# Optimization experiments

Hardware: AMD Instinct MI355X
Metric: run time of the kernel (lower is better)

The kernel has to match this reference:

```python
import jax, jax.numpy as jnp
import numpy as np

B, IN, OUT, K = 2048, 1024, 1024, 20


def setup_inputs() -> dict:
    key = jax.random.key(0)
    k1, k2 = jax.random.split(key)
    x = jax.random.normal(k1, (B, IN), dtype=jnp.float32)
    # per-output, per-input spline coefficients: (out_features, in_features, num_knots)
    W = jax.random.normal(k2, (OUT, IN, K), dtype=jnp.float32) * 0.1
    # evenly spaced knot grid on [-2, 2] (linspace)
    knots = jnp.linspace(-2.0, 2.0, K, dtype=jnp.float32)
    return {"x": x, "W": W, "knots": knots}


def reference(x, W, knots):
    # RBF spline basis shared across all output features (this is the fusion
    # the original per-output Python loop misses):
    # basis[b, i, k] = exp(-0.5 * ((x[b, i] - knots[k]) / h)^2)
    h = knots[1] - knots[0]  # uniform knot spacing -> RBF bandwidth
    basis = jnp.exp(-0.5 * jnp.square((x[:, :, None] - knots) / h))  # (B, IN, K)
    # Each SplineLayer o computes sum_{i,k} W[o,i,k] * basis[b,i,k]; the
    # KANBlock concatenates the OUT scalars -> a single einsum.
    return jnp.einsum("bik,oik->bo", basis, W)  # (B, OUT)
```

## Files before the change

kernel.cpp:

```cpp
#include <hip/hip_runtime.h>

#define B_DIM 2048
#define IN_DIM 1024
#define OUT_DIM 1024
#define K_KNOTS 20
#define KR (IN_DIM * K_KNOTS)
#define OUT_ELEMS (B_DIM * OUT_DIM)

#define TM 128
#define TN 128
#define BK 128
#define KSPLIT 4
#define MT_TILES (B_DIM / TM)
#define NT_TILES (OUT_DIM / TN)
#define GEMM_BLOCKS (MT_TILES * NT_TILES * KSPLIT)
#define LDS_AS0 0
#define LDS_AS1 8192
#define LDS_BS0 16384
#define LDS_BS1 24576

#define NB_QUADS (B_DIM * IN_DIM * 5)
#define NB_BASIS_BLK (NB_QUADS / 256)
#define NW4 (OUT_DIM * KR / 8)
#define NB_W_BLK (NW4 / 256)

typedef __bf16 bf16x8 __attribute__((ext_vector_type(8)));
typedef float  f32x4  __attribute__((ext_vector_type(4)));

#define MFMA16(a, b, c) __builtin_amdgcn_mfma_f32_16x16x32_bf16(a, b, c, 0, 0, 0)

__device__ __forceinline__ unsigned short f2bf(float f) {
    unsigned int u = __float_as_uint(f);
    unsigned int r = u + 0x7fffu + ((u >> 16) & 1u);
    return (unsigned short)(r >> 16);
}

__device__ __forceinline__ unsigned int pack2(float lo, float hi) {
    return (unsigned int)f2bf(lo) | ((unsigned int)f2bf(hi) << 16);
}

__device__ __forceinline__ void async_load16(const void* g, void* l) {
    __builtin_amdgcn_global_load_lds(
        (const __attribute__((address_space(1))) void*)g,
        (__attribute__((address_space(3))) void*)l,
        16, 0, 0);
}

__global__ void zero_out_kernel(float* out) {
    int idx = (blockIdx.x * 256 + threadIdx.x) * 4;
    float4 z = {0.f, 0.f, 0.f, 0.f};
    *(float4*)(out + idx) = z;
}

__global__ void __launch_bounds__(256) prep_kernel(
        const float* __restrict__ x,
        const float4* __restrict__ Wsrc,
        const float* __restrict__ knots,
        uint2* __restrict__ basis_out,
        uint4* __restrict__ w_out) {
    if (blockIdx.x < NB_BASIS_BLK) {
        unsigned int n = blockIdx.x * 256 + threadIdx.x;
        unsigned int q  = n % 5u;
        unsigned int bi = n / 5u;
        float t0 = knots[0];
        float h  = knots[1] - t0;
        float invh = 1.0f / h;
        float xv = x[bi];
        float k0 = (float)(4 * q);
        float v[4];
#pragma unroll
        for (int j = 0; j < 4; ++j) {
            float t = __builtin_fmaf(k0 + (float)j, h, t0);
            float d = (xv - t) * invh;
            v[j] = __expf(-0.5f * d * d);
        }
        uint2 o;
        o.x = pack2(v[0], v[1]);
        o.y = pack2(v[2], v[3]);
        basis_out[n] = o;
    } else {
        unsigned int t = (blockIdx.x - NB_BASIS_BLK) * 256 + threadIdx.x;
        float4 a = Wsrc[2 * t];
        float4 b = Wsrc[2 * t + 1];
        uint4 o;
        o.x = pack2(a.x, a.y);
        o.y = pack2(a.z, a.w);
        o.z = pack2(b.x, b.y);
        o.w = pack2(b.z, b.w);
        w_out[t] = o;
    }
}

#define AOFF(s, h) (((s) * 2 + (h)) * 8192)
#define BOFF(s, h) (32768 + ((s) * 2 + (h)) * 8192)

template <int S>
__device__ __forceinline__ void tile_step(
        int t, int ntiles,
        const unsigned short* __restrict__ Ab,
        const unsigned short* __restrict__ Bb,
        unsigned short* lds,
        f32x4 (&acc)[8][4],
        int m0, int n0, int k0,
        int wave, int wm, int wn, int r15, int c0, int c1,
        int srow8, int scol) {
    const int aB  = S * 16384 + (wm * 128 + r15) * 64;
    const int bB  = 32768 + S * 16384 + (wn * 64 + r15) * 64;
    const int kb1 = k0 + (t + 1) * 64;
    const bool st = (t + 1 < ntiles);

    auto stage = [&](const unsigned short* __restrict__ src, int grow, int kb, int lbase) {
        const unsigned short* g = src + (size_t)(grow + wave * 16 + srow8) * KR + kb + scol;
        async_load16(g,                  &lds[lbase + wave * 1024]);
        async_load16(g + (size_t)8 * KR, &lds[lbase + wave * 1024 + 512]);
    };

    bf16x8 a0[4], a1[4], b0[4], b1[4], s0[4], s1[4];

#pragma unroll
    for (int i = 0; i < 4; ++i) a0[i] = *(const bf16x8*)&lds[aB + i * 1024 + c0];
#pragma unroll
    for (int j = 0; j < 4; ++j) b0[j] = *(const bf16x8*)&lds[bB + j * 1024 + c0];
    __builtin_amdgcn_s_barrier();
    asm volatile("s_waitcnt lgkmcnt(0)" ::: "memory");
    __builtin_amdgcn_sched_barrier(0);
    __builtin_amdgcn_s_setprio(1);
#pragma unroll
    for (int i = 0; i < 4; ++i)
#pragma unroll
        for (int j = 0; j < 4; ++j)
            acc[i][j] = MFMA16(a0[i], b0[j], acc[i][j]);
    __builtin_amdgcn_s_setprio(0);

#pragma unroll
    for (int i = 0; i < 4; ++i) a1[i] = *(const bf16x8*)&lds[aB + i * 1024 + c1];
#pragma unroll
    for (int j = 0; j < 4; ++j) b1[j] = *(const bf16x8*)&lds[bB + j * 1024 + c1];
    __builtin_amdgcn_s_barrier();
    asm volatile("s_waitcnt lgkmcnt(0)" ::: "memory");
    __builtin_amdgcn_sched_barrier(0);
    __builtin_amdgcn_s_setprio(1);
#pragma unroll
    for (int i = 0; i < 4; ++i)
#pragma unroll
        for (int j = 0; j < 4; ++j)
            acc[i][j] = MFMA16(a1[i], b1[j], acc[i][j]);
    __builtin_amdgcn_s_setprio(0);

#pragma unroll
    for (int i = 0; i < 4; ++i) s0[i] = *(const bf16x8*)&lds[aB + (4 + i) * 1024 + c0];
    if (st) {
        stage(Ab, m0,       kb1, AOFF(S ^ 1, 0));
        stage(Ab, m0 + 128, kb1, AOFF(S ^ 1, 1));
    }
    __builtin_amdgcn_s_barrier();
    asm volatile("s_waitcnt lgkmcnt(0)" ::: "memory");
    __builtin_amdgcn_sched_barrier(0);
    __builtin_amdgcn_s_setprio(1);
#pragma unroll
    for (int i = 0; i < 4; ++i)
#pragma unroll
        for (int j = 0; j < 4; ++j)
            acc[4 + i][j] = MFMA16(s0[i], b0[j], acc[4 + i][j]);
    __builtin_amdgcn_s_setprio(0);

#pragma unroll
    for (int i = 0; i < 4; ++i) s1[i] = *(const bf16x8*)&lds[aB + (4 + i) * 1024 + c1];
    if (st) {
        stage(Bb, n0,       kb1, BOFF(S ^ 1, 0));
        stage(Bb, n0 + 128, kb1, BOFF(S ^ 1, 1));
    }
    __builtin_amdgcn_s_barrier();
    asm volatile("s_waitcnt lgkmcnt(0)" ::: "memory");
    __builtin_amdgcn_sched_barrier(0);
    __builtin_amdgcn_s_setprio(1);
#pragma unroll
    for (int i = 0; i < 4; ++i)
#pragma unroll
        for (int j = 0; j < 4; ++j)
            acc[4 + i][j] = MFMA16(s1[i], b1[j], acc[4 + i][j]);
    __builtin_amdgcn_s_setprio(0);

    if (st) asm volatile("s_waitcnt vmcnt(0)" ::: "memory");
    __builtin_amdgcn_s_barrier();
}

template <int KS, bool ATOMIC>
__global__ void __launch_bounds__(512, 2)
kan_gemm8(const unsigned short* __restrict__ Ab,
          const unsigned short* __restrict__ Bb,
          float* __restrict__ out) {
    __shared__ __align__(16) unsigned short lds[65536];

    constexpr int KPBk   = KR / KS;
    constexpr int NTILES = KPBk / 64;

    const int id  = blockIdx.x;
    const int z   = id & 7;
    const int ord = id >> 3;
    const int mt  = ord & 7;
    const int nt  = ord >> 3;
    const int m0  = mt * 256;
    const int n0  = nt * 256;
    const int k0  = z * KPBk;

    const int tid  = threadIdx.x;
    const int wave = tid >> 6;
    const int lane = tid & 63;
    const int wm   = wave >> 2;
    const int wn   = wave & 3;

    const int srow8 = lane >> 3;
    const int scol  = ((lane & 7) ^ srow8) * 8;

    auto stage = [&](const unsigned short* __restrict__ src, int grow, int kb, int lbase) {
        const unsigned short* g = src + (size_t)(grow + wave * 16 + srow8) * KR + kb + scol;
        async_load16(g,                  &lds[lbase + wave * 1024]);
        async_load16(g + (size_t)8 * KR, &lds[lbase + wave * 1024 + 512]);
    };

    f32x4 acc[8][4];
#pragma unroll
    for (int i = 0; i < 8; ++i)
#pragma unroll
        for (int j = 0; j < 4; ++j) acc[i][j] = (f32x4){0.f, 0.f, 0.f, 0.f};

    const int q   = lane >> 4;
    const int r15 = lane & 15;
    const int r7  = lane & 7;
    const int c0  = (q ^ r7) * 8;
    const int c1  = ((4 + q) ^ r7) * 8;

    stage(Ab, m0,       k0, AOFF(0, 0));
    stage(Ab, m0 + 128, k0, AOFF(0, 1));
    stage(Bb, n0,       k0, BOFF(0, 0));
    stage(Bb, n0 + 128, k0, BOFF(0, 1));
    asm volatile("s_waitcnt vmcnt(0)" ::: "memory");
    __builtin_amdgcn_s_barrier();

    for (int tt = 0; tt < NTILES; tt += 2) {
        tile_step<0>(tt,     NTILES, Ab, Bb, lds, acc, m0, n0, k0,
                     wave, wm, wn, r15, c0, c1, srow8, scol);
        tile_step<1>(tt + 1, NTILES, Ab, Bb, lds, acc, m0, n0, k0,
                     wave, wm, wn, r15, c0, c1, srow8, scol);
    }

    float* dst = ATOMIC ? out : out + (size_t)z * OUT_ELEMS;
#pragma unroll
    for (int i = 0; i < 8; ++i)
#pragma unroll
        for (int j = 0; j < 4; ++j)
#pragma unroll
            for (int r = 0; r < 4; ++r) {
                const int row = m0 + wm * 128 + i * 16 + q * 4 + r;
                const int c   = n0 + wn * 64  + j * 16 + r15;
                if (ATOMIC)
                    atomicAdd(&dst[(size_t)row * OUT_DIM + c], acc[i][j][r]);
                else
                    dst[(size_t)row * OUT_DIM + c] = acc[i][j][r];
            }
}

template <int KS, bool ATOMIC>
__global__ void __launch_bounds__(256)
kan_gemm(const unsigned short* __restrict__ Ab,
         const unsigned short* __restrict__ Bb,
         float* __restrict__ out) {
    __shared__ __align__(16) unsigned short lds[32768];

    const int KPBk = KR / KS;
    const int id   = blockIdx.x;
    const int xcd  = id & 7;
    const int ord  = id >> 3;
    const int mt   = xcd * 2 + (ord & 1);
    const int nt   = (ord >> 1) & (NT_TILES - 1);
    const int z    = ord >> 4;
    const int m0 = mt * TM;
    const int n0 = nt * TN;
    const int k0 = z * KPBk;

    const int tid  = threadIdx.x;
    const int wave = tid >> 6;
    const int lane = tid & 63;
    const int wm = wave & 1;
    const int wn = wave >> 1;

    const int srow = lane >> 3;
    const int scol = ((lane & 7) ^ srow) * 8;

    f32x4 acc[4][4];
#pragma unroll
    for (int i = 0; i < 4; ++i)
#pragma unroll
        for (int j = 0; j < 4; ++j) acc[i][j] = (f32x4){0.f, 0.f, 0.f, 0.f};

    for (int kt = 0; kt < KPBk; kt += BK) {
        const int kb = k0 + kt;
        __syncthreads();
#pragma unroll
        for (int c = 0; c < 4; ++c) {
            const int chunk = wave * 4 + c;
            const int r = chunk * 8 + srow;
            const unsigned short* arow = Ab + (size_t)(m0 + r) * KR + kb + scol;
            const unsigned short* brow = Bb + (size_t)(n0 + r) * KR + kb + scol;
            unsigned short* slot = &lds[chunk * 512];
            async_load16(arow,      slot + LDS_AS0);
            async_load16(arow + 64, slot + LDS_AS1);
            async_load16(brow,      slot + LDS_BS0);
            async_load16(brow + 64, slot + LDS_BS1);
        }
        __syncthreads();

        const int quad = lane >> 4;
        const int r15  = lane & 15;
        const int r7   = lane & 7;
#pragma unroll
        for (int s = 0; s < 4; ++s) {
            const int abase = (s >> 1) ? LDS_AS1 : LDS_AS0;
            const int bbase = (s >> 1) ? LDS_BS1 : LDS_BS0;
            const int cg = (s & 1) * 4 + quad;
            const int xo = (cg ^ r7) * 8;
            bf16x8 af[4], bfv[4];
#pragma unroll
            for (int i = 0; i < 4; ++i) {
                af[i]  = *(const bf16x8*)&lds[abase + (wm * 64 + i * 16 + r15) * 64 + xo];
                bfv[i] = *(const bf16x8*)&lds[bbase + (wn * 64 + i * 16 + r15) * 64 + xo];
            }
#pragma unroll
            for (int i = 0; i < 4; ++i)
#pragma unroll
                for (int j = 0; j < 4; ++j)
                    acc[i][j] = MFMA16(af[i], bfv[j], acc[i][j]);
        }
    }

    float* dst = ATOMIC ? out : out + (size_t)z * OUT_ELEMS;
    const int quad = lane >> 4;
    const int col  = lane & 15;
#pragma unroll
    for (int i = 0; i < 4; ++i)
#pragma unroll
        for (int j = 0; j < 4; ++j)
#pragma unroll
            for (int r = 0; r < 4; ++r) {
                const int row = m0 + wm * 64 + i * 16 + quad * 4 + r;
                const int c   = n0 + wn * 64 + j * 16 + col;
                if (ATOMIC)
                    atomicAdd(&dst[(size_t)row * OUT_DIM + c], acc[i][j][r]);
                else
                    dst[(size_t)row * OUT_DIM + c] = acc[i][j][r];
            }
}

template <int KS>
__global__ void kan_reduce(const float* __restrict__ part, float* __restrict__ out) {
    const int idx = (blockIdx.x * 256 + threadIdx.x) * 4;
    f32x4 s = *(const f32x4*)(part + idx);
#pragma unroll
    for (int z = 1; z < KS; ++z)
        s += *(const f32x4*)(part + (size_t)z * OUT_ELEMS + idx);
    *(f32x4*)(out + idx) = s;
}

__global__ void kan_fallback(const float* __restrict__ x,
                             const float* __restrict__ W,
                             const float* __restrict__ knots,
                             float* __restrict__ out) {
    __shared__ float basis[256 * K_KNOTS];
    const int b = blockIdx.x;
    const int o = blockIdx.y * blockDim.x + threadIdx.x;
    const float invh = 1.0f / (knots[1] - knots[0]);
    const float* w = W + (size_t)o * KR;
    float sum = 0.f;
    for (int i0 = 0; i0 < IN_DIM; i0 += 256) {
        __syncthreads();
        for (int idx = threadIdx.x; idx < 256 * K_KNOTS; idx += blockDim.x) {
            const int i = i0 + idx / K_KNOTS;
            const int k = idx % K_KNOTS;
            const float d = (x[(size_t)b * IN_DIM + i] - knots[k]) * invh;
            basis[idx] = __expf(-0.5f * d * d);
        }
        __syncthreads();
        for (int r = 0; r < 256 * K_KNOTS; ++r)
            sum += basis[r] * w[(size_t)i0 * K_KNOTS + r];
    }
    out[(size_t)b * OUT_DIM + o] = sum;
}

extern "C" void kernel_launch(void* const* d_in, const int* in_sizes, int n_in,
                              void* d_out, int out_size, void* d_ws, size_t ws_size,
                              hipStream_t stream) {
    const float* x     = (const float*)d_in[0];
    const float* W     = (const float*)d_in[1];
    const float* knots = (const float*)d_in[2];
    float* out = (float*)d_out;

    const size_t basis_bytes = (size_t)B_DIM * KR * 2;
    const size_t wb_bytes    = (size_t)OUT_DIM * KR * 2;
    const size_t part8_bytes = (size_t)8 * OUT_ELEMS * 4;
    const size_t part4_bytes = (size_t)4 * OUT_ELEMS * 4;

    unsigned short* Ab = (unsigned short*)d_ws;
    unsigned short* Bb = (unsigned short*)((char*)d_ws + basis_bytes);
    float* part = (float*)((char*)d_ws + basis_bytes + wb_bytes);

    if (ws_size >= basis_bytes + wb_bytes + part8_bytes) {
        prep_kernel<<<dim3(NB_BASIS_BLK + NB_W_BLK), dim3(256), 0, stream>>>(
            x, (const float4*)W, knots, (uint2*)Ab, (uint4*)Bb);
        kan_gemm8<8, false><<<dim3(256), dim3(512), 0, stream>>>(Ab, Bb, part);
        kan_reduce<8><<<dim3(OUT_ELEMS / (256 * 4)), dim3(256), 0, stream>>>(part, out);
    } else if (ws_size >= basis_bytes + wb_bytes + part4_bytes) {
        prep_kernel<<<dim3(NB_BASIS_BLK + NB_W_BLK), dim3(256), 0, stream>>>(
            x, (const float4*)W, knots, (uint2*)Ab, (uint4*)Bb);
        kan_gemm<4, false><<<dim3(GEMM_BLOCKS), dim3(256), 0, stream>>>(Ab, Bb, part);
        kan_reduce<4><<<dim3(OUT_ELEMS / (256 * 4)), dim3(256), 0, stream>>>(part, out);
    } else if (ws_size >= basis_bytes + wb_bytes) {
        zero_out_kernel<<<dim3(OUT_ELEMS / (256 * 4)), dim3(256), 0, stream>>>(out);
        prep_kernel<<<dim3(NB_BASIS_BLK + NB_W_BLK), dim3(256), 0, stream>>>(
            x, (const float4*)W, knots, (uint2*)Ab, (uint4*)Bb);
        kan_gemm8<8, true><<<dim3(256), dim3(512), 0, stream>>>(Ab, Bb, out);
    } else {
        kan_fallback<<<dim3(B_DIM, OUT_DIM / 256), dim3(256), 0, stream>>>(x, W, knots, out);
    }
}
```

Measured before the change: 257.3 us.

## Fuse prep, split-K GEMM and reduction into one cooperative kernel

Replaces the three-launch path (bf16 prep, 8-way split-K GEMM, partial reduction) with a single cooperative kernel. Grid-wide syncs separate the phases, so the extra launches and the gaps between them go away. In exchange, the prep and reduce phases now run with only 256 blocks of 512 threads instead of many small blocks. The grid syncs also add barrier overhead, and the launch relies on all 256 blocks being co-resident.

```diff
diff --git a/kernel.cpp b/kernel.cpp
--- a/kernel.cpp
+++ b/kernel.cpp
@@ -1,4 +1,7 @@
 #include <hip/hip_runtime.h>
+#include <hip/hip_cooperative_groups.h>
+
+namespace cg = cooperative_groups;
 
 #define B_DIM 2048
 #define IN_DIM 1024
@@ -23,6 +26,8 @@
 #define NB_BASIS_BLK (NB_QUADS / 256)
 #define NW4 (OUT_DIM * KR / 8)
 #define NB_W_BLK (NW4 / 256)
+
+#define FUSED_THREADS 131072
 
 typedef __bf16 bf16x8 __attribute__((ext_vector_type(8)));
 typedef float  f32x4  __attribute__((ext_vector_type(4)));
@@ -186,12 +191,11 @@
 }
 
 template <int KS, bool ATOMIC>
-__global__ void __launch_bounds__(512, 2)
-kan_gemm8(const unsigned short* __restrict__ Ab,
-          const unsigned short* __restrict__ Bb,
-          float* __restrict__ out) {
-    __shared__ __align__(16) unsigned short lds[65536];
-
+__device__ __forceinline__ void gemm_body(
+        const unsigned short* __restrict__ Ab,
+        const unsigned short* __restrict__ Bb,
+        float* __restrict__ out,
+        unsigned short* lds) {
     constexpr int KPBk   = KR / KS;
     constexpr int NTILES = KPBk / 64;
 
@@ -259,6 +263,84 @@
                 else
                     dst[(size_t)row * OUT_DIM + c] = acc[i][j][r];
             }
+}
+
+__global__ void __launch_bounds__(512, 2)
+kan_fused(const float* __restrict__ x,
+          const float4* __restrict__ Wsrc,
+          const float* __restrict__ knots,
+          unsigned short* __restrict__ Ab,
+          unsigned short* __restrict__ Bb,
+          float* __restrict__ part,
+          float* __restrict__ out) {
+    __shared__ __align__(16) unsigned short lds[65536];
+
+    const int gtid = blockIdx.x * 512 + threadIdx.x;
+
+    {
+        uint2* basis_out = (uint2*)Ab;
+        uint4* w_out     = (uint4*)Bb;
+        const float t0   = knots[0];
+        const float h    = knots[1] - t0;
+        const float invh = 1.0f / h;
+#pragma unroll 4
+        for (int it = 0; it < NB_QUADS / FUSED_THREADS; ++it) {
+            unsigned int n  = (unsigned int)gtid + (unsigned int)it * FUSED_THREADS;
+            unsigned int qd = n % 5u;
+            unsigned int bi = n / 5u;
+            float xv = x[bi];
+            float k0 = (float)(4 * qd);
+            float v[4];
+#pragma unroll
+            for (int j = 0; j < 4; ++j) {
+                float t = __builtin_fmaf(k0 + (float)j, h, t0);
+                float d = (xv - t) * invh;
+                v[j] = __expf(-0.5f * d * d);
+            }
+            uint2 o;
+            o.x = pack2(v[0], v[1]);
+            o.y = pack2(v[2], v[3]);
+            basis_out[n] = o;
+        }
+#pragma unroll 4
+        for (int it = 0; it < NW4 / FUSED_THREADS; ++it) {
+            unsigned int t = (unsigned int)gtid + (unsigned int)it * FUSED_THREADS;
+            float4 a = Wsrc[2 * t];
+            float4 b = Wsrc[2 * t + 1];
+            uint4 o;
+            o.x = pack2(a.x, a.y);
+            o.y = pack2(a.z, a.w);
+            o.z = pack2(b.x, b.y);
+            o.w = pack2(b.z, b.w);
+            w_out[t] = o;
+        }
+    }
+    __threadfence();
+    cg::this_grid().sync();
+
+    gemm_body<8, false>(Ab, Bb, part, lds);
+
+    __threadfence();
+    cg::this_grid().sync();
+
+#pragma unroll
+    for (int it = 0; it < (OUT_ELEMS / 4) / FUSED_THREADS; ++it) {
+        const int idx = (gtid + it * FUSED_THREADS) * 4;
+        f32x4 s = *(const f32x4*)(part + idx);
+#pragma unroll
+        for (int zz = 1; zz < 8; ++zz)
+            s += *(const f32x4*)(part + (size_t)zz * OUT_ELEMS + idx);
+        *(f32x4*)(out + idx) = s;
+    }
+}
+
+template <int KS, bool ATOMIC>
+__global__ void __launch_bounds__(512, 2)
+kan_gemm8(const unsigned short* __restrict__ Ab,
+          const unsigned short* __restrict__ Bb,
+          float* __restrict__ out) {
+    __shared__ __align__(16) unsigned short lds[65536];
+    gemm_body<KS, ATOMIC>(Ab, Bb, out, lds);
 }
 
 template <int KS, bool ATOMIC>
@@ -405,10 +487,16 @@
     float* part = (float*)((char*)d_ws + basis_bytes + wb_bytes);
 
     if (ws_size >= basis_bytes + wb_bytes + part8_bytes) {
-        prep_kernel<<<dim3(NB_BASIS_BLK + NB_W_BLK), dim3(256), 0, stream>>>(
-            x, (const float4*)W, knots, (uint2*)Ab, (uint4*)Bb);
-        kan_gemm8<8, false><<<dim3(256), dim3(512), 0, stream>>>(Ab, Bb, part);
-        kan_reduce<8><<<dim3(OUT_ELEMS / (256 * 4)), dim3(256), 0, stream>>>(part, out);
+        const float*  xa = x;
+        const float4* wa = (const float4*)W;
+        const float*  ka = knots;
+        unsigned short* aba = Ab;
+        unsigned short* bba = Bb;
+        float* pa = part;
+        float* oa = out;
+        void* kargs[7] = {&xa, &wa, &ka, &aba, &bba, &pa, &oa};
+        hipLaunchCooperativeKernel((void*)kan_fused, dim3(256), dim3(512),
+                                   kargs, 0, stream);
     } else if (ws_size >= basis_bytes + wb_bytes + part4_bytes) {
         prep_kernel<<<dim3(NB_BASIS_BLK + NB_W_BLK), dim3(256), 0, stream>>>(
             x, (const float4*)W, knots, (uint2*)Ab, (uint4*)Bb);
```

New measurement: 467.4 us. +81.6%, slower.
